# Kernel tuning notes

Measured on AMD Instinct MI355X. Metric: run time of the kernel, lower is better.

Reference implementation:

```python
import jax, jax.numpy as jnp
import numpy as np

B, T, I, H = 32, 8192, 1, 256
OS_FACTOR = 1.5  # delay_near=1, delay_far=2, alpha=0.5, allpass coeff=(1-a)/(1+a)=1/3


def setup_inputs() -> dict:
    key = jax.random.key(0)
    ks = jax.random.split(key, 5)
    s = 1.0 / np.sqrt(H)  # torch LSTMCell init scale
    x = jax.random.normal(ks[0], (B, T, I), jnp.float32)
    W_ih = jax.random.normal(ks[1], (4 * H, I), jnp.float32) * s
    W_hh = jax.random.normal(ks[2], (4 * H, H), jnp.float32) * s
    b_ih = jax.random.normal(ks[3], (4 * H,), jnp.float32) * s
    b_hh = jax.random.normal(ks[4], (4 * H,), jnp.float32) * s
    return {"x": x, "W_ih": W_ih, "W_hh": W_hh, "b_ih": b_ih, "b_hh": b_hh}


def reference(x, W_ih, W_hh, b_ih, b_hh):
    # APDL_RNN forward with LSTMCell, h=None, os_factor=1.5.
    delay_near = int(np.floor(OS_FACTOR))          # 1
    alpha = OS_FACTOR - delay_near                 # 0.5
    coeff = (1.0 - alpha) / (1.0 + alpha)          # 1/3
    Bsz = x.shape[0]
    Hh = W_hh.shape[1]
    S = 2 * Hh  # LSTM state = concat(h, c)

    # Precompute input projection for all timesteps: [B, T, 4H]
    xg = jnp.einsum('bti,gi->btg', x, W_ih) + b_ih

    zero = jnp.zeros((Bsz, S), x.dtype)
    # carry: (state[i-1], state[i-2], ap_state) -- zero-init matches h=None
    init = (zero, zero, zero)

    def step(carry, xg_t):
        s1, s2, ap = carry
        # first-order allpass interpolated delayed state
        ap = coeff * (s1 - ap) + s2
        h, c = ap[:, :Hh], ap[:, Hh:]
        gates = xg_t + h @ W_hh.T + b_hh  # [B, 4H]
        i_g, f_g, g_g, o_g = jnp.split(gates, 4, axis=-1)  # torch gate order
        c_new = jax.nn.sigmoid(f_g) * c + jax.nn.sigmoid(i_g) * jnp.tanh(g_g)
        h_new = jax.nn.sigmoid(o_g) * jnp.tanh(c_new)
        s_new = jnp.concatenate([h_new, c_new], axis=-1)
        return (s_new, s1, ap), s_new

    (_, _, ap_final), states = jax.lax.scan(step, init, jnp.swapaxes(xg, 0, 1))
    states = jnp.swapaxes(states, 0, 1)  # [B, T, 2H]
    y = states[..., :Hh]
    return y, states[..., :Hh], states[..., Hh:], ap_final
```

## Files before the change

### kernel.cpp

```cpp
#include <hip/hip_runtime.h>


#define Bn 32
#define Tn 8192
#define Hn 256
#define HPAD 136

typedef float floatx4 __attribute__((ext_vector_type(4)));

static constexpr float kCoeff = 1.0f / 3.0f;

__device__ __forceinline__ float sigf(float x) {
  return __builtin_amdgcn_rcpf(1.0f + __expf(-x));
}
__device__ __forceinline__ float tanhf_fast(float x) {
  return 1.0f - 2.0f * __builtin_amdgcn_rcpf(1.0f + __expf(2.0f * x));
}
__device__ __forceinline__ float pick4(int d, float v0, float v1, float v2, float v3) {
  float r = (d == 0) ? v0 : v1;
  r = (d == 2) ? v2 : r;
  r = (d == 3) ? v3 : r;
  return r;
}

__global__ void init_ws(unsigned int* ws) {
  int i = blockIdx.x * 256 + threadIdx.x;
  if (i < 32768) ws[i] = 0;
}

#define LOADW(i) floatx4 w##i = *(const floatx4*)(wrow + 4 * (i))
#define PINW(i) asm volatile("" : "+v"(w##i))
#define ACC8(i, j, K)                                        \
  {                                                          \
    floatx4 p = *(const floatx4*)&hsp[(K)];                  \
    floatx4 q = *(const floatx4*)&hsp[(K) + 4];              \
    a0 = fmaf(w##i[0], p[0], a0); a1 = fmaf(w##i[1], p[1], a1); \
    a2 = fmaf(w##i[2], p[2], a2); a3 = fmaf(w##i[3], p[3], a3); \
    a4 = fmaf(w##j[0], q[0], a4); a5 = fmaf(w##j[1], q[1], a5); \
    a6 = fmaf(w##j[2], q[2], a6); a7 = fmaf(w##j[3], q[3], a7); \
  }

__global__ __launch_bounds__(512, 2) void apdl_rnn(
    const float* __restrict__ x, const float* __restrict__ W_ih,
    const float* __restrict__ W_hh, const float* __restrict__ b_ih,
    const float* __restrict__ b_hh, float* __restrict__ out,
    unsigned long long* __restrict__ pub) {
  const int bid = blockIdx.x;
  const int w = bid >> 5;
  const int b = bid & 31;
  const int tid = (int)threadIdx.x;
  const int hf = tid & 1;
  const int p = tid >> 1;
  const int g = p & 3;
  const int ul = p >> 2;
  const int u = w * 64 + ul;
  const int row = g * Hn + u;

  __shared__ __align__(16) float xs[Tn];
  __shared__ __align__(16) float hs[2 * HPAD];

  for (int i = tid; i < Tn; i += 512) xs[i] = x[b * Tn + i];

  const float* wrow = W_hh + row * Hn + hf * 128;
  LOADW(0);  LOADW(1);  LOADW(2);  LOADW(3);  LOADW(4);  LOADW(5);  LOADW(6);  LOADW(7);
  LOADW(8);  LOADW(9);  LOADW(10); LOADW(11); LOADW(12); LOADW(13); LOADW(14); LOADW(15);
  LOADW(16); LOADW(17); LOADW(18); LOADW(19); LOADW(20); LOADW(21); LOADW(22); LOADW(23);
  LOADW(24); LOADW(25); LOADW(26); LOADW(27); LOADW(28); LOADW(29); LOADW(30); LOADW(31);
  asm volatile("s_waitcnt vmcnt(0)" ::: "memory");
  PINW(0);  PINW(1);  PINW(2);  PINW(3);  PINW(4);  PINW(5);  PINW(6);  PINW(7);
  PINW(8);  PINW(9);  PINW(10); PINW(11); PINW(12); PINW(13); PINW(14); PINW(15);
  PINW(16); PINW(17); PINW(18); PINW(19); PINW(20); PINW(21); PINW(22); PINW(23);
  PINW(24); PINW(25); PINW(26); PINW(27); PINW(28); PINW(29); PINW(30); PINW(31);

  const float wih = W_ih[row];
  const float bias = b_ih[row] + b_hh[row];
  const float* hsp = hs + hf * HPAD;

  unsigned long long* mypub = pub + b * 2 * Hn;

  float s1_h = 0.f, s1_c = 0.f, ap_h = 0.f, ap_c = 0.f;

  for (int t = 0; t < Tn; ++t) {
    if (tid < Hn) {
      const int idx = tid + ((tid >> 7) << 3);
      if (t == 0) {
        hs[idx] = 0.f;
      } else {
        unsigned long long pk;
        do {
          pk = __hip_atomic_load(mypub + (t & 1) * Hn + tid, __ATOMIC_RELAXED,
                                 __HIP_MEMORY_SCOPE_AGENT);
        } while ((unsigned int)pk != (unsigned int)t);
        hs[idx] = __uint_as_float((unsigned int)(pk >> 32));
      }
    }
    __syncthreads();

    float a0 = 0.f, a1 = 0.f, a2 = 0.f, a3 = 0.f;
    float a4 = 0.f, a5 = 0.f, a6 = 0.f, a7 = 0.f;
    ACC8(0, 1, 0);     ACC8(2, 3, 8);     ACC8(4, 5, 16);    ACC8(6, 7, 24);
    ACC8(8, 9, 32);    ACC8(10, 11, 40);  ACC8(12, 13, 48);  ACC8(14, 15, 56);
    ACC8(16, 17, 64);  ACC8(18, 19, 72);  ACC8(20, 21, 80);  ACC8(22, 23, 88);
    ACC8(24, 25, 96);  ACC8(26, 27, 104); ACC8(28, 29, 112); ACC8(30, 31, 120);
    float half = ((a0 + a1) + (a2 + a3)) + ((a4 + a5) + (a6 + a7));
    float dot = half + __shfl_xor(half, 1);
    float raw = dot + xs[t] * wih + bias;

    float act = (g == 2) ? tanhf_fast(raw) : sigf(raw);
    float v1 = __shfl_xor(act, 2);
    float v2 = __shfl_xor(act, 4);
    float v3 = __shfl_xor(act, 6);
    float ai = pick4(g,     act, v1, v2, v3);
    float af = pick4(g ^ 1, act, v1, v2, v3);
    float ag = pick4(g ^ 2, act, v1, v2, v3);
    float ao = pick4(g ^ 3, act, v1, v2, v3);

    float c_new = af * ap_c + ai * ag;
    float h_new = ao * tanhf_fast(c_new);

    if (t < Tn - 1) {
      float nh = kCoeff * (h_new - ap_h) + s1_h;
      float nc = kCoeff * (c_new - ap_c) + s1_c;
      s1_h = h_new; s1_c = c_new; ap_h = nh; ap_c = nc;
      if (g == 3 && hf == 0) {
        unsigned long long pk =
            ((unsigned long long)__float_as_uint(nh) << 32) | (unsigned int)(t + 1);
        __hip_atomic_store(mypub + ((t + 1) & 1) * Hn + u, pk, __ATOMIC_RELAXED,
                           __HIP_MEMORY_SCOPE_AGENT);
      }
    } else {
      if (g == 0 && hf == 0)      out[201326592 + b * 512 + u] = ap_h;
      else if (g == 1 && hf == 0) out[201326592 + b * 512 + 256 + u] = ap_c;
    }

    int o = (b * Tn + t) * Hn + u;
    if (hf == 0) {
      if (g == 0)      out[o] = h_new;
      else if (g == 2) out[67108864 + o] = h_new;
      else if (g == 1) out[134217728 + o] = c_new;
    }

    __syncthreads();
  }
}

extern "C" void kernel_launch(void* const* d_in, const int* in_sizes, int n_in,
                              void* d_out, int out_size, void* d_ws, size_t ws_size,
                              hipStream_t stream) {
  const float* x = (const float*)d_in[0];
  const float* W_ih = (const float*)d_in[1];
  const float* W_hh = (const float*)d_in[2];
  const float* b_ih = (const float*)d_in[3];
  const float* b_hh = (const float*)d_in[4];
  float* out = (float*)d_out;
  unsigned long long* pub = (unsigned long long*)d_ws;

  init_ws<<<128, 256, 0, stream>>>((unsigned int*)d_ws);
  apdl_rnn<<<128, 512, 0, stream>>>(x, W_ih, W_hh, b_ih, b_hh, out, pub);
}
```

Measured before the change: 11.30 ms.

## Publish raw gate preactivations in fp16 and compute cell update redundantly per block

Each block now publishes the four gate pre-activations of its units, packed as fp16 with a step tag, instead of the final interpolated hidden value. Every block polls all 256 units with 16-byte cache-bypassing loads and recomputes the LSTM cell and allpass state locally for the whole hidden vector. The shared h buffer is double-buffered, which removes the second barrier per step. The aim is to shorten the cross-block critical path, removing gate shuffles and one sync per step, at the cost of redundant nonlinearity work and fp16 rounding of the gates, which may hurt accuracy.

```diff
diff --git a/kernel.cpp b/kernel.cpp
--- a/kernel.cpp
+++ b/kernel.cpp
@@ -1,4 +1,5 @@
 #include <hip/hip_runtime.h>
+#include <hip/hip_fp16.h>
 
 
 #define Bn 32
@@ -7,6 +8,7 @@
 #define HPAD 136
 
 typedef float floatx4 __attribute__((ext_vector_type(4)));
+typedef unsigned int uintx4 __attribute__((ext_vector_type(4)));
 
 static constexpr float kCoeff = 1.0f / 3.0f;
 
@@ -16,29 +18,38 @@
 __device__ __forceinline__ float tanhf_fast(float x) {
   return 1.0f - 2.0f * __builtin_amdgcn_rcpf(1.0f + __expf(2.0f * x));
 }
-__device__ __forceinline__ float pick4(int d, float v0, float v1, float v2, float v3) {
-  float r = (d == 0) ? v0 : v1;
-  r = (d == 2) ? v2 : r;
-  r = (d == 3) ? v3 : r;
-  return r;
-}
 
 __global__ void init_ws(unsigned int* ws) {
   int i = blockIdx.x * 256 + threadIdx.x;
-  if (i < 32768) ws[i] = 0;
+  if (i < 65536) ws[i] = 0;
 }
 
 #define LOADW(i) floatx4 w##i = *(const floatx4*)(wrow + 4 * (i))
 #define PINW(i) asm volatile("" : "+v"(w##i))
-#define ACC8(i, j, K)                                        \
-  {                                                          \
-    floatx4 p = *(const floatx4*)&hsp[(K)];                  \
-    floatx4 q = *(const floatx4*)&hsp[(K) + 4];              \
+#define ACC8(i, j, K)                                           \
+  {                                                             \
+    floatx4 p = *(const floatx4*)&hsp[(K)];                     \
+    floatx4 q = *(const floatx4*)&hsp[(K) + 4];                 \
     a0 = fmaf(w##i[0], p[0], a0); a1 = fmaf(w##i[1], p[1], a1); \
     a2 = fmaf(w##i[2], p[2], a2); a3 = fmaf(w##i[3], p[3], a3); \
     a4 = fmaf(w##j[0], q[0], a4); a5 = fmaf(w##j[1], q[1], a5); \
     a6 = fmaf(w##j[2], q[2], a6); a7 = fmaf(w##j[3], q[3], a7); \
   }
+
+__device__ __forceinline__ uintx4 poll16(const unsigned long long* a8, unsigned want) {
+  uintx4 va, vb, res;
+  asm volatile("global_load_dwordx4 %0, %1, off sc0 sc1" : "=v"(va) : "v"(a8));
+  for (;;) {
+    asm volatile("global_load_dwordx4 %0, %1, off sc0 sc1" : "=v"(vb) : "v"(a8));
+    asm volatile("s_waitcnt vmcnt(1)" : "+v"(va) :: "memory");
+    if (va.x == want && va.z == want) { res = va; break; }
+    asm volatile("global_load_dwordx4 %0, %1, off sc0 sc1" : "=v"(va) : "v"(a8));
+    asm volatile("s_waitcnt vmcnt(1)" : "+v"(vb) :: "memory");
+    if (vb.x == want && vb.z == want) { res = vb; break; }
+  }
+  asm volatile("s_waitcnt vmcnt(0)" : "+v"(va), "+v"(vb) :: "memory");
+  return res;
+}
 
 __global__ __launch_bounds__(512, 2) void apdl_rnn(
     const float* __restrict__ x, const float* __restrict__ W_ih,
@@ -52,12 +63,11 @@
   const int hf = tid & 1;
   const int p = tid >> 1;
   const int g = p & 3;
-  const int ul = p >> 2;
-  const int u = w * 64 + ul;
-  const int row = g * Hn + u;
+  const int uG = w * 64 + (p >> 2);
+  const int row = g * Hn + uG;
 
   __shared__ __align__(16) float xs[Tn];
-  __shared__ __align__(16) float hs[2 * HPAD];
+  __shared__ __align__(16) float hs2[2][2 * HPAD];
 
   for (int i = tid; i < Tn; i += 512) xs[i] = x[b * Tn + i];
 
@@ -74,73 +84,70 @@
 
   const float wih = W_ih[row];
   const float bias = b_ih[row] + b_hh[row];
-  const float* hsp = hs + hf * HPAD;
 
-  unsigned long long* mypub = pub + b * 2 * Hn;
+  unsigned long long* mypub = pub + (size_t)b * 2 * Hn * 2;
 
-  float s1_h = 0.f, s1_c = 0.f, ap_h = 0.f, ap_c = 0.f;
+  float s1h = 0.f, s1c = 0.f, aph = 0.f, apc = 0.f;
 
-  for (int t = 0; t < Tn; ++t) {
-    if (tid < Hn) {
-      const int idx = tid + ((tid >> 7) << 3);
-      if (t == 0) {
-        hs[idx] = 0.f;
-      } else {
-        unsigned long long pk;
-        do {
-          pk = __hip_atomic_load(mypub + (t & 1) * Hn + tid, __ATOMIC_RELAXED,
-                                 __HIP_MEMORY_SCOPE_AGENT);
-        } while ((unsigned int)pk != (unsigned int)t);
-        hs[idx] = __uint_as_float((unsigned int)(pk >> 32));
+  for (int t = 0;; ++t) {
+    if (t == 0) {
+      if (tid < Hn) hs2[0][tid + ((tid >> 7) << 3)] = 0.f;
+    } else {
+      if (tid < Hn) {
+        const int ur = tid;
+        uintx4 pk = poll16(mypub + ((size_t)(t & 1) * Hn + ur) * 2, (unsigned)t);
+        float gi = __half2float(__ushort_as_half((unsigned short)(pk.y & 0xffff)));
+        float gf = __half2float(__ushort_as_half((unsigned short)(pk.y >> 16)));
+        float gg = __half2float(__ushort_as_half((unsigned short)(pk.w & 0xffff)));
+        float go = __half2float(__ushort_as_half((unsigned short)(pk.w >> 16)));
+        float ai = sigf(gi), af = sigf(gf), ag = tanhf_fast(gg), ao = sigf(go);
+        float c_new = af * apc + ai * ag;
+        float h_new = ao * tanhf_fast(c_new);
+        if (t < Tn) {
+          float nh = kCoeff * (h_new - aph) + s1h;
+          float nc = kCoeff * (c_new - apc) + s1c;
+          s1h = h_new; s1c = c_new; aph = nh; apc = nc;
+          hs2[t & 1][ur + ((ur >> 7) << 3)] = nh;
+        }
+        if ((ur >> 6) == w) {
+          int o = (b * Tn + (t - 1)) * Hn + ur;
+          out[o] = h_new;
+          out[67108864 + o] = h_new;
+          out[134217728 + o] = c_new;
+          if (t == Tn) {
+            out[201326592 + b * 512 + ur] = aph;
+            out[201326592 + b * 512 + 256 + ur] = apc;
+          }
+        }
       }
+      if (t == Tn) break;
     }
     __syncthreads();
 
+    const float* hsp = &hs2[t & 1][hf * HPAD];
     float a0 = 0.f, a1 = 0.f, a2 = 0.f, a3 = 0.f;
     float a4 = 0.f, a5 = 0.f, a6 = 0.f, a7 = 0.f;
     ACC8(0, 1, 0);     ACC8(2, 3, 8);     ACC8(4, 5, 16);    ACC8(6, 7, 24);
     ACC8(8, 9, 32);    ACC8(10, 11, 40);  ACC8(12, 13, 48);  ACC8(14, 15, 56);
     ACC8(16, 17, 64);  ACC8(18, 19, 72);  ACC8(20, 21, 80);  ACC8(22, 23, 88);
     ACC8(24, 25, 96);  ACC8(26, 27, 104); ACC8(28, 29, 112); ACC8(30, 31, 120);
-    float half = ((a0 + a1) + (a2 + a3)) + ((a4 + a5) + (a6 + a7));
-    float dot = half + __shfl_xor(half, 1);
+    float half_ = ((a0 + a1) + (a2 + a3)) + ((a4 + a5) + (a6 + a7));
+    float dot = half_ + __shfl_xor(half_, 1);
     float raw = dot + xs[t] * wih + bias;
 
-    float act = (g == 2) ? tanhf_fast(raw) : sigf(raw);
-    float v1 = __shfl_xor(act, 2);
-    float v2 = __shfl_xor(act, 4);
-    float v3 = __shfl_xor(act, 6);
-    float ai = pick4(g,     act, v1, v2, v3);
-    float af = pick4(g ^ 1, act, v1, v2, v3);
-    float ag = pick4(g ^ 2, act, v1, v2, v3);
-    float ao = pick4(g ^ 3, act, v1, v2, v3);
-
-    float c_new = af * ap_c + ai * ag;
-    float h_new = ao * tanhf_fast(c_new);
-
-    if (t < Tn - 1) {
-      float nh = kCoeff * (h_new - ap_h) + s1_h;
-      float nc = kCoeff * (c_new - ap_c) + s1_c;
-      s1_h = h_new; s1_c = c_new; ap_h = nh; ap_c = nc;
-      if (g == 3 && hf == 0) {
-        unsigned long long pk =
-            ((unsigned long long)__float_as_uint(nh) << 32) | (unsigned int)(t + 1);
-        __hip_atomic_store(mypub + ((t + 1) & 1) * Hn + u, pk, __ATOMIC_RELAXED,
-                           __HIP_MEMORY_SCOPE_AGENT);
-      }
-    } else {
-      if (g == 0 && hf == 0)      out[201326592 + b * 512 + u] = ap_h;
-      else if (g == 1 && hf == 0) out[201326592 + b * 512 + 256 + u] = ap_c;
+    float orow = __shfl_xor(raw, 2);
+    unsigned lo16 = (unsigned)__half_as_ushort(__float2half(raw));
+    unsigned hi16 = (unsigned)__half_as_ushort(__float2half(orow));
+    unsigned p01 = lo16 | (hi16 << 16);
+    unsigned p23 = __shfl_xor(p01, 4);
+    if ((tid & 7) == 0) {
+      unsigned tag = (unsigned)(t + 1);
+      unsigned long long* ps = mypub + ((size_t)((t + 1) & 1) * Hn + uG) * 2;
+      __hip_atomic_store(ps, (unsigned long long)tag | ((unsigned long long)p01 << 32),
+                         __ATOMIC_RELAXED, __HIP_MEMORY_SCOPE_AGENT);
+      __hip_atomic_store(ps + 1, (unsigned long long)tag | ((unsigned long long)p23 << 32),
+                         __ATOMIC_RELAXED, __HIP_MEMORY_SCOPE_AGENT);
     }
-
-    int o = (b * Tn + t) * Hn + u;
-    if (hf == 0) {
-      if (g == 0)      out[o] = h_new;
-      else if (g == 2) out[67108864 + o] = h_new;
-      else if (g == 1) out[134217728 + o] = c_new;
-    }
-
-    __syncthreads();
   }
 }
 
@@ -155,6 +162,6 @@
   float* out = (float*)d_out;
   unsigned long long* pub = (unsigned long long*)d_ws;
 
-  init_ws<<<128, 256, 0, stream>>>((unsigned int*)d_ws);
+  init_ws<<<256, 256, 0, stream>>>((unsigned int*)d_ws);
   apdl_rnn<<<128, 512, 0, stream>>>(x, W_ih, W_hh, b_ih, b_hh, out, pub);
 }
```

Result: slower. 16.51 ms (+46.1%).

## Double-buffer shared hidden state, write local slice directly, pipeline polling loads

Applied to the files above, without the earlier changes.

Makes the shared hidden-state buffer double-buffered by timestep parity, which lets the second __syncthreads per step be removed. Each block now writes its own 64 hidden units straight into shared memory and polls only the units produced by the other three blocks. Polling keeps four outstanding agent-scope loads in flight so the flag is seen sooner. The goal is less cross-block latency on the serial recurrence. The cost is extra shared memory and more reliance on the parity buffer to avoid read/write races.

```diff
diff --git a/kernel.cpp b/kernel.cpp
--- a/kernel.cpp
+++ b/kernel.cpp
@@ -22,6 +22,9 @@
   r = (d == 3) ? v3 : r;
   return r;
 }
+__device__ __forceinline__ unsigned long long ld_agent(const unsigned long long* p) {
+  return __hip_atomic_load(p, __ATOMIC_RELAXED, __HIP_MEMORY_SCOPE_AGENT);
+}
 
 __global__ void init_ws(unsigned int* ws) {
   int i = blockIdx.x * 256 + threadIdx.x;
@@ -30,10 +33,10 @@
 
 #define LOADW(i) floatx4 w##i = *(const floatx4*)(wrow + 4 * (i))
 #define PINW(i) asm volatile("" : "+v"(w##i))
-#define ACC8(i, j, K)                                        \
-  {                                                          \
-    floatx4 p = *(const floatx4*)&hsp[(K)];                  \
-    floatx4 q = *(const floatx4*)&hsp[(K) + 4];              \
+#define ACC8(i, j, K)                                           \
+  {                                                             \
+    floatx4 p = *(const floatx4*)&hsp[(K)];                     \
+    floatx4 q = *(const floatx4*)&hsp[(K) + 4];                 \
     a0 = fmaf(w##i[0], p[0], a0); a1 = fmaf(w##i[1], p[1], a1); \
     a2 = fmaf(w##i[2], p[2], a2); a3 = fmaf(w##i[3], p[3], a3); \
     a4 = fmaf(w##j[0], q[0], a4); a5 = fmaf(w##j[1], q[1], a5); \
@@ -57,7 +60,7 @@
   const int row = g * Hn + u;
 
   __shared__ __align__(16) float xs[Tn];
-  __shared__ __align__(16) float hs[2 * HPAD];
+  __shared__ __align__(16) float hs2[2][2 * HPAD];
 
   for (int i = tid; i < Tn; i += 512) xs[i] = x[b * Tn + i];
 
@@ -74,28 +77,39 @@
 
   const float wih = W_ih[row];
   const float bias = b_ih[row] + b_hh[row];
-  const float* hsp = hs + hf * HPAD;
 
   unsigned long long* mypub = pub + b * 2 * Hn;
+
+  const bool poller = (tid < Hn) && ((tid >> 6) != w);
 
   float s1_h = 0.f, s1_c = 0.f, ap_h = 0.f, ap_c = 0.f;
 
   for (int t = 0; t < Tn; ++t) {
-    if (tid < Hn) {
-      const int idx = tid + ((tid >> 7) << 3);
-      if (t == 0) {
-        hs[idx] = 0.f;
-      } else {
-        unsigned long long pk;
-        do {
-          pk = __hip_atomic_load(mypub + (t & 1) * Hn + tid, __ATOMIC_RELAXED,
-                                 __HIP_MEMORY_SCOPE_AGENT);
-        } while ((unsigned int)pk != (unsigned int)t);
-        hs[idx] = __uint_as_float((unsigned int)(pk >> 32));
+    if (t == 0) {
+      if (tid < Hn) hs2[0][tid + ((tid >> 7) << 3)] = 0.f;
+    } else if (poller) {
+      const unsigned long long* pa = mypub + (t & 1) * Hn + tid;
+      const unsigned want = (unsigned)t;
+      unsigned long long v0 = ld_agent(pa);
+      unsigned long long v1 = ld_agent(pa);
+      unsigned long long v2 = ld_agent(pa);
+      unsigned long long v3 = ld_agent(pa);
+      unsigned long long pk;
+      for (;;) {
+        if ((unsigned)v0 == want) { pk = v0; break; }
+        v0 = ld_agent(pa);
+        if ((unsigned)v1 == want) { pk = v1; break; }
+        v1 = ld_agent(pa);
+        if ((unsigned)v2 == want) { pk = v2; break; }
+        v2 = ld_agent(pa);
+        if ((unsigned)v3 == want) { pk = v3; break; }
+        v3 = ld_agent(pa);
       }
+      hs2[t & 1][tid + ((tid >> 7) << 3)] = __uint_as_float((unsigned int)(pk >> 32));
     }
     __syncthreads();
 
+    const float* hsp = &hs2[t & 1][hf * HPAD];
     float a0 = 0.f, a1 = 0.f, a2 = 0.f, a3 = 0.f;
     float a4 = 0.f, a5 = 0.f, a6 = 0.f, a7 = 0.f;
     ACC8(0, 1, 0);     ACC8(2, 3, 8);     ACC8(4, 5, 16);    ACC8(6, 7, 24);
@@ -127,6 +141,7 @@
             ((unsigned long long)__float_as_uint(nh) << 32) | (unsigned int)(t + 1);
         __hip_atomic_store(mypub + ((t + 1) & 1) * Hn + u, pk, __ATOMIC_RELAXED,
                            __HIP_MEMORY_SCOPE_AGENT);
+        hs2[(t + 1) & 1][u + ((u >> 7) << 3)] = nh;
       }
     } else {
       if (g == 0 && hf == 0)      out[201326592 + b * 512 + u] = ap_h;
@@ -139,8 +154,6 @@
       else if (g == 2) out[67108864 + o] = h_new;
       else if (g == 1) out[134217728 + o] = c_new;
     }
-
-    __syncthreads();
   }
 }
 
```

New measurement: 14.51 ms. 1.28x slower.
